# Performance work log

Hardware: AMD Instinct MI355X
Metric: run time of the kernel (lower is better)

Reference implementation:

```python
import jax, jax.numpy as jnp
import numpy as np

C = 128          # in_channels
NODE_NUM = 8192  # number of unique source nodes this step
D = 64           # max_member_num (fixed degree -> neighbor_bool all True)
E = NODE_NUM * D # total gathered neighbor slots
N_TOTAL = 200000 # total nodes in graph
NEG_SLOPE = 0.2


def setup_inputs() -> dict:
    key = jax.random.key(0)
    ks = jax.random.split(key, 8)
    node_features = jax.random.normal(ks[0], (N_TOTAL, C), jnp.float32)
    memory = jax.random.normal(ks[1], (N_TOTAL, C), jnp.float32)
    sc = 1.0 / np.sqrt(C)
    W_max = jax.random.normal(ks[2], (C, C), jnp.float32) * sc
    b_max = jnp.zeros((C,), jnp.float32)
    W_score = jax.random.normal(ks[3], (2 * C, 1), jnp.float32) * (1.0 / np.sqrt(2 * C))
    b_score = jnp.zeros((1,), jnp.float32)
    W_fit = jax.random.normal(ks[4], (C, 1), jnp.float32) * sc
    b_fit = jnp.zeros((1,), jnp.float32)
    neighbors = jax.random.randint(ks[5], (E,), 0, N_TOTAL)  # gathered neighbor node ids
    seg = jnp.repeat(jnp.arange(NODE_NUM), D)                # index_source_nodes (segment ids)
    return dict(node_features=node_features, memory=memory, W_max=W_max, b_max=b_max,
                W_score=W_score, b_score=b_score, W_fit=W_fit, b_fit=b_fit,
                neighbors=neighbors, seg=seg)


def reference(node_features, memory, W_max, b_max, W_score, b_score, W_fit, b_fit, neighbors, seg):
    # gather: features + detached memory per neighbor slot  [E, C]
    nbr = node_features[neighbors] + jax.lax.stop_gradient(memory[neighbors])
    # scatter_max per source node, then linear + re-gather duplication
    max_feature = jax.ops.segment_max(nbr, seg, num_segments=NODE_NUM)      # [node_num, C]
    max_lin = max_feature @ W_max + b_max                                    # [node_num, C]
    dup = max_lin[seg]                                                       # [E, C]
    # attention score over concat(center_max, neighbor)
    s = jnp.concatenate([dup, nbr], axis=-1) @ W_score + b_score             # [E, 1]
    s = jnp.where(s >= 0, s, NEG_SLOPE * s)                                  # leaky_relu
    # segment softmax over neighbors of each source node
    smax = jax.ops.segment_max(s, seg, num_segments=NODE_NUM)[seg]
    ex = jnp.exp(s - smax)
    denom = jax.ops.segment_sum(ex, seg, num_segments=NODE_NUM)[seg]
    score = ex / denom                                                       # [E, 1]
    # masked scatter into fixed [node_num, max_member_num] tensor (full mask -> reshape)
    score_tensor = score.reshape(NODE_NUM, D)
    # scatter_add pooling of score-weighted neighbor features
    cluster_feature = jax.ops.segment_sum(nbr * score, seg, num_segments=NODE_NUM)  # [node_num, C]
    # community fitness via linear score calculator + sigmoid
    fitness = jax.nn.sigmoid(cluster_feature @ W_fit + b_fit).reshape(-1)    # [node_num]
    return cluster_feature, score_tensor, fitness
```

## Files before the change

kernel.cpp:

```cpp
#include <hip/hip_runtime.h>
#include <hip/hip_fp16.h>
#include <math.h>

#define C_DIM 128
#define DEG 64
#define NEG_SLOPE 0.2f

typedef float nfloat4 __attribute__((ext_vector_type(4)));

__global__ __launch_bounds__(256)
void fuse_sum_half_kernel(const nfloat4* __restrict__ nf4,
                          const nfloat4* __restrict__ mem4,
                          nfloat4* __restrict__ sumh, long n8,
                          const float* __restrict__ W_max,
                          const float* __restrict__ b_max,
                          const float* __restrict__ W_score,
                          const float* __restrict__ b_score,
                          float* __restrict__ combo) {
    const long stride = (long)gridDim.x * 256;
    for (long i = (long)blockIdx.x * 256 + threadIdx.x; i < n8; i += stride) {
        const nfloat4 a0 = __builtin_nontemporal_load(nf4 + 2 * i);
        const nfloat4 a1 = __builtin_nontemporal_load(nf4 + 2 * i + 1);
        const nfloat4 b0 = __builtin_nontemporal_load(mem4 + 2 * i);
        const nfloat4 b1 = __builtin_nontemporal_load(mem4 + 2 * i + 1);
        const nfloat4 s0 = a0 + b0;
        const nfloat4 s1 = a1 + b1;
        __half2 h[4];
        h[0] = __floats2half2_rn(s0.x, s0.y);
        h[1] = __floats2half2_rn(s0.z, s0.w);
        h[2] = __floats2half2_rn(s1.x, s1.y);
        h[3] = __floats2half2_rn(s1.z, s1.w);
        sumh[i] = *(const nfloat4*)h;
    }
    if (blockIdx.x == 0) {
        const int c = threadIdx.x;
        __shared__ float red[C_DIM];
        if (c < C_DIM) {
            float acc = 0.f;
            #pragma unroll 4
            for (int k = 0; k < C_DIM; ++k)
                acc += W_max[c * C_DIM + k] * W_score[k];
            combo[c] = acc;
            red[c] = b_max[c] * W_score[c];
        }
        __syncthreads();
        for (int off = 64; off > 0; off >>= 1) {
            if (c < off) red[c] += red[c + off];
            __syncthreads();
        }
        if (c == 0) combo[C_DIM] = red[0] + b_score[0];
    }
}

__global__ __launch_bounds__(256)
void detector_half_kernel(const float4* __restrict__ sum4,
                          const float* __restrict__ W_score,
                          const float* __restrict__ W_fit,
                          const float* __restrict__ b_fit,
                          const int* __restrict__ neighbors,
                          const float* __restrict__ combo,
                          float* __restrict__ out_cf,
                          float* __restrict__ out_score,
                          float* __restrict__ out_fit) {
    __shared__ float4 red4[256][2];
    __shared__ float  chan[C_DIM];
    __shared__ float  s_raw[DEG];
    __shared__ float  sc[DEG];

    const int tid = threadIdx.x;
    const int n   = blockIdx.x;
    const int q   = tid & 15;
    const int g   = tid >> 4;

    const int4 nb = ((const int4*)(neighbors + n * DEG))[g];
    const int ids[4] = {nb.x, nb.y, nb.z, nb.w};

    const float4 wsb0 = ((const float4*)(W_score + C_DIM))[2 * q];
    const float4 wsb1 = ((const float4*)(W_score + C_DIM))[2 * q + 1];

    float4 vh[4];
    float mx[8];
    #pragma unroll
    for (int k = 0; k < 8; ++k) mx[k] = -INFINITY;

    #pragma unroll
    for (int i = 0; i < 4; ++i) {
        const long node = ids[i];
        const float4 hv = sum4[node * 16 + q];
        vh[i] = hv;
        const __half2* hp = (const __half2*)&hv;
        const float2 f0 = __half22float2(hp[0]);
        const float2 f1 = __half22float2(hp[1]);
        const float2 f2 = __half22float2(hp[2]);
        const float2 f3 = __half22float2(hp[3]);
        mx[0] = fmaxf(mx[0], f0.x); mx[1] = fmaxf(mx[1], f0.y);
        mx[2] = fmaxf(mx[2], f1.x); mx[3] = fmaxf(mx[3], f1.y);
        mx[4] = fmaxf(mx[4], f2.x); mx[5] = fmaxf(mx[5], f2.y);
        mx[6] = fmaxf(mx[6], f3.x); mx[7] = fmaxf(mx[7], f3.y);
        float p = f0.x * wsb0.x + f0.y * wsb0.y + f1.x * wsb0.z + f1.y * wsb0.w
                + f2.x * wsb1.x + f2.y * wsb1.y + f3.x * wsb1.z + f3.y * wsb1.w;
        p += __shfl_xor(p, 1);
        p += __shfl_xor(p, 2);
        p += __shfl_xor(p, 4);
        p += __shfl_xor(p, 8);
        if (q == 0) s_raw[g * 4 + i] = p;
    }
    asm volatile("" ::: "memory");

    red4[tid][0] = make_float4(mx[0], mx[1], mx[2], mx[3]);
    red4[tid][1] = make_float4(mx[4], mx[5], mx[6], mx[7]);
    __syncthreads();

    const float* rp = (const float*)red4;
    if (tid < C_DIM) {
        const int ch = tid >> 3;
        const int k  = tid & 7;
        float f = rp[(0 * 16 + ch) * 8 + k];
        #pragma unroll
        for (int g2 = 1; g2 < 16; ++g2)
            f = fmaxf(f, rp[(g2 * 16 + ch) * 8 + k]);
        chan[tid] = f * combo[tid];
    }
    __syncthreads();

    if (tid < DEG) {
        float t1 = chan[tid] + chan[tid + 64];
        #pragma unroll
        for (int msk = 1; msk <= 32; msk <<= 1)
            t1 += __shfl_xor(t1, msk);
        t1 += combo[C_DIM];
        float s = t1 + s_raw[tid];
        s = (s >= 0.f) ? s : NEG_SLOPE * s;
        float m = s;
        #pragma unroll
        for (int msk = 1; msk <= 32; msk <<= 1)
            m = fmaxf(m, __shfl_xor(m, msk));
        const float ex = __expf(s - m);
        float d = ex;
        #pragma unroll
        for (int msk = 1; msk <= 32; msk <<= 1)
            d += __shfl_xor(d, msk);
        const float sv = ex / d;
        sc[tid] = sv;
        out_score[n * DEG + tid] = sv;
    }
    __syncthreads();

    float acc[8] = {0.f, 0.f, 0.f, 0.f, 0.f, 0.f, 0.f, 0.f};
    #pragma unroll
    for (int i = 0; i < 4; ++i) {
        const float w = sc[g * 4 + i];
        const __half2* hp = (const __half2*)&vh[i];
        const float2 f0 = __half22float2(hp[0]);
        const float2 f1 = __half22float2(hp[1]);
        const float2 f2 = __half22float2(hp[2]);
        const float2 f3 = __half22float2(hp[3]);
        acc[0] += f0.x * w; acc[1] += f0.y * w;
        acc[2] += f1.x * w; acc[3] += f1.y * w;
        acc[4] += f2.x * w; acc[5] += f2.y * w;
        acc[6] += f3.x * w; acc[7] += f3.y * w;
    }
    __syncthreads();
    red4[tid][0] = make_float4(acc[0], acc[1], acc[2], acc[3]);
    red4[tid][1] = make_float4(acc[4], acc[5], acc[6], acc[7]);
    __syncthreads();

    if (tid < C_DIM) {
        const int ch = tid >> 3;
        const int k  = tid & 7;
        float f = 0.f;
        #pragma unroll
        for (int g2 = 0; g2 < 16; ++g2)
            f += rp[(g2 * 16 + ch) * 8 + k];
        out_cf[(long)n * C_DIM + tid] = f;
        chan[tid] = f * W_fit[tid];
    }
    __syncthreads();

    if (tid < DEG) {
        float t = chan[tid] + chan[tid + 64];
        #pragma unroll
        for (int msk = 1; msk <= 32; msk <<= 1)
            t += __shfl_xor(t, msk);
        if (tid == 0)
            out_fit[n] = 1.f / (1.f + __expf(-(t + b_fit[0])));
    }
}

__global__ void precompute_kernel(const float* __restrict__ W_max,
                                  const float* __restrict__ b_max,
                                  const float* __restrict__ W_score,
                                  const float* __restrict__ b_score,
                                  float* __restrict__ combo) {
    const int c = threadIdx.x;
    float acc = 0.f;
    for (int k = 0; k < C_DIM; ++k)
        acc += W_max[c * C_DIM + k] * W_score[k];
    combo[c] = acc;
    __shared__ float red[C_DIM];
    red[c] = b_max[c] * W_score[c];
    __syncthreads();
    for (int off = 64; off > 0; off >>= 1) {
        if (c < off) red[c] += red[c + off];
        __syncthreads();
    }
    if (c == 0) combo[C_DIM] = red[0] + b_score[0];
}

__global__ __launch_bounds__(256)
void detector_f32_kernel(const float* __restrict__ nf,
                         const float* __restrict__ mem,
                         const float* __restrict__ W_score,
                         const float* __restrict__ W_fit,
                         const float* __restrict__ b_fit,
                         const int* __restrict__ neighbors,
                         const float* __restrict__ combo,
                         float* __restrict__ out_cf,
                         float* __restrict__ out_score,
                         float* __restrict__ out_fit) {
    __shared__ float4 red[256];
    __shared__ float  s_raw[DEG];
    __shared__ float  sc[DEG];
    __shared__ float  t1_sh;

    const int tid = threadIdx.x;
    const int n   = blockIdx.x;
    const int q   = tid & 31;
    const int g   = tid >> 5;

    const int4* nb4 = (const int4*)(neighbors + n * DEG + g * 8);
    const int4 nba = nb4[0];
    const int4 nbb = nb4[1];
    const int ids[8] = {nba.x, nba.y, nba.z, nba.w, nbb.x, nbb.y, nbb.z, nbb.w};
    const float4 wsb = ((const float4*)(W_score + C_DIM))[q];
    const float4* nf4  = (const float4*)nf;
    const float4* mem4 = (const float4*)mem;

    float4 v[8];
    float4 mx = make_float4(-INFINITY, -INFINITY, -INFINITY, -INFINITY);
    #pragma unroll
    for (int i = 0; i < 8; ++i) {
        const long node = ids[i];
        float4 vv = nf4[node * 32 + q];
        const float4 b = mem4[node * 32 + q];
        vv.x += b.x; vv.y += b.y; vv.z += b.z; vv.w += b.w;
        v[i] = vv;
        mx.x = fmaxf(mx.x, vv.x); mx.y = fmaxf(mx.y, vv.y);
        mx.z = fmaxf(mx.z, vv.z); mx.w = fmaxf(mx.w, vv.w);
        float p = vv.x * wsb.x + vv.y * wsb.y + vv.z * wsb.z + vv.w * wsb.w;
        p += __shfl_xor(p, 1); p += __shfl_xor(p, 2); p += __shfl_xor(p, 4);
        p += __shfl_xor(p, 8); p += __shfl_xor(p, 16);
        if (q == 0) s_raw[g * 8 + i] = p;
    }
    asm volatile("" ::: "memory");
    red[tid] = mx;
    __syncthreads();
    if (tid < 32) {
        float4 f = red[tid];
        #pragma unroll
        for (int r = 1; r < 8; ++r) {
            const float4 o = red[tid + 32 * r];
            f.x = fmaxf(f.x, o.x); f.y = fmaxf(f.y, o.y);
            f.z = fmaxf(f.z, o.z); f.w = fmaxf(f.w, o.w);
        }
        const float4 wc = ((const float4*)combo)[tid];
        float t1 = f.x * wc.x + f.y * wc.y + f.z * wc.z + f.w * wc.w;
        t1 += __shfl_xor(t1, 1); t1 += __shfl_xor(t1, 2); t1 += __shfl_xor(t1, 4);
        t1 += __shfl_xor(t1, 8); t1 += __shfl_xor(t1, 16);
        if (tid == 0) t1_sh = t1 + combo[C_DIM];
    }
    __syncthreads();
    if (tid < DEG) {
        float s = t1_sh + s_raw[tid];
        s = (s >= 0.f) ? s : NEG_SLOPE * s;
        float m = s;
        #pragma unroll
        for (int msk = 1; msk <= 32; msk <<= 1) m = fmaxf(m, __shfl_xor(m, msk));
        const float ex = __expf(s - m);
        float d = ex;
        #pragma unroll
        for (int msk = 1; msk <= 32; msk <<= 1) d += __shfl_xor(d, msk);
        const float sv = ex / d;
        sc[tid] = sv;
        out_score[n * DEG + tid] = sv;
    }
    __syncthreads();
    float4 acc = make_float4(0.f, 0.f, 0.f, 0.f);
    #pragma unroll
    for (int i = 0; i < 8; ++i) {
        const float w = sc[g * 8 + i];
        acc.x += v[i].x * w; acc.y += v[i].y * w;
        acc.z += v[i].z * w; acc.w += v[i].w * w;
    }
    red[tid] = acc;
    __syncthreads();
    if (tid < 32) {
        float4 f = red[tid];
        #pragma unroll
        for (int r = 1; r < 8; ++r) {
            const float4 o = red[tid + 32 * r];
            f.x += o.x; f.y += o.y; f.z += o.z; f.w += o.w;
        }
        ((float4*)(out_cf + (long)n * C_DIM))[tid] = f;
        const float4 wf = ((const float4*)W_fit)[tid];
        float fp = f.x * wf.x + f.y * wf.y + f.z * wf.z + f.w * wf.w;
        fp += __shfl_xor(fp, 1); fp += __shfl_xor(fp, 2); fp += __shfl_xor(fp, 4);
        fp += __shfl_xor(fp, 8); fp += __shfl_xor(fp, 16);
        if (tid == 0)
            out_fit[n] = 1.f / (1.f + __expf(-(fp + b_fit[0])));
    }
}

extern "C" void kernel_launch(void* const* d_in, const int* in_sizes, int n_in,
                              void* d_out, int out_size, void* d_ws, size_t ws_size,
                              hipStream_t stream) {
    const float* node_features = (const float*)d_in[0];
    const float* memory        = (const float*)d_in[1];
    const float* W_max         = (const float*)d_in[2];
    const float* b_max         = (const float*)d_in[3];
    const float* W_score       = (const float*)d_in[4];
    const float* b_score       = (const float*)d_in[5];
    const float* W_fit         = (const float*)d_in[6];
    const float* b_fit         = (const float*)d_in[7];
    const int*   neighbors     = (const int*)d_in[8];

    const long n_elem = (long)in_sizes[0];
    const int  nodes  = in_sizes[8] / DEG;
    const long n8     = n_elem / 8;

    float* combo = (float*)d_ws;
    __half* sumh = (__half*)(combo + 512);
    const size_t need = 512 * sizeof(float) + (size_t)n_elem * sizeof(__half);

    float* out_cf    = (float*)d_out;
    float* out_score = out_cf + (long)nodes * C_DIM;
    float* out_fit   = out_score + (long)nodes * DEG;

    if (ws_size >= need) {
        fuse_sum_half_kernel<<<2048, 256, 0, stream>>>(
            (const nfloat4*)node_features, (const nfloat4*)memory,
            (nfloat4*)sumh, n8, W_max, b_max, W_score, b_score, combo);
        detector_half_kernel<<<nodes, 256, 0, stream>>>(
            (const float4*)sumh, W_score, W_fit, b_fit, neighbors, combo,
            out_cf, out_score, out_fit);
    } else {
        precompute_kernel<<<1, C_DIM, 0, stream>>>(W_max, b_max, W_score,
                                                   b_score, combo);
        detector_f32_kernel<<<nodes, 256, 0, stream>>>(
            node_features, memory, W_score, W_fit, b_fit, neighbors, combo,
            out_cf, out_score, out_fit);
    }
}
```

Before: 263.3 us.

## Process two source nodes per block and widen the fp16 pre-sum kernel

The detector kernel now handles two source nodes per 256-thread block, issuing all eight gathers per thread before any compute and combining the reduction stages for both nodes, so fewer barriers are paid per node. The pre-sum kernel drops its grid-stride loop and launches one thread per 16 floats, each doing eight nontemporal loads and two 16-byte stores. The aim is more memory-level parallelism in the random gather and less per-node synchronisation. It costs more registers and shared memory per block, and the fast path now requires an even node count and an element count divisible by 16.

```diff
diff --git a/kernel.cpp b/kernel.cpp
--- a/kernel.cpp
+++ b/kernel.cpp
@@ -11,26 +11,35 @@
 __global__ __launch_bounds__(256)
 void fuse_sum_half_kernel(const nfloat4* __restrict__ nf4,
                           const nfloat4* __restrict__ mem4,
-                          nfloat4* __restrict__ sumh, long n8,
+                          nfloat4* __restrict__ sumh4, long n16,
                           const float* __restrict__ W_max,
                           const float* __restrict__ b_max,
                           const float* __restrict__ W_score,
                           const float* __restrict__ b_score,
                           float* __restrict__ combo) {
-    const long stride = (long)gridDim.x * 256;
-    for (long i = (long)blockIdx.x * 256 + threadIdx.x; i < n8; i += stride) {
-        const nfloat4 a0 = __builtin_nontemporal_load(nf4 + 2 * i);
-        const nfloat4 a1 = __builtin_nontemporal_load(nf4 + 2 * i + 1);
-        const nfloat4 b0 = __builtin_nontemporal_load(mem4 + 2 * i);
-        const nfloat4 b1 = __builtin_nontemporal_load(mem4 + 2 * i + 1);
-        const nfloat4 s0 = a0 + b0;
-        const nfloat4 s1 = a1 + b1;
-        __half2 h[4];
-        h[0] = __floats2half2_rn(s0.x, s0.y);
-        h[1] = __floats2half2_rn(s0.z, s0.w);
-        h[2] = __floats2half2_rn(s1.x, s1.y);
-        h[3] = __floats2half2_rn(s1.z, s1.w);
-        sumh[i] = *(const nfloat4*)h;
+    const long idx = (long)blockIdx.x * 256 + threadIdx.x;
+    if (idx < n16) {
+        const long b = idx * 4;
+        nfloat4 a0 = __builtin_nontemporal_load(nf4 + b);
+        nfloat4 a1 = __builtin_nontemporal_load(nf4 + b + 1);
+        nfloat4 a2 = __builtin_nontemporal_load(nf4 + b + 2);
+        nfloat4 a3 = __builtin_nontemporal_load(nf4 + b + 3);
+        nfloat4 m0 = __builtin_nontemporal_load(mem4 + b);
+        nfloat4 m1 = __builtin_nontemporal_load(mem4 + b + 1);
+        nfloat4 m2 = __builtin_nontemporal_load(mem4 + b + 2);
+        nfloat4 m3 = __builtin_nontemporal_load(mem4 + b + 3);
+        const nfloat4 s0 = a0 + m0, s1 = a1 + m1, s2 = a2 + m2, s3 = a3 + m3;
+        __half2 h0[4], h1[4];
+        h0[0] = __floats2half2_rn(s0.x, s0.y);
+        h0[1] = __floats2half2_rn(s0.z, s0.w);
+        h0[2] = __floats2half2_rn(s1.x, s1.y);
+        h0[3] = __floats2half2_rn(s1.z, s1.w);
+        h1[0] = __floats2half2_rn(s2.x, s2.y);
+        h1[1] = __floats2half2_rn(s2.z, s2.w);
+        h1[2] = __floats2half2_rn(s3.x, s3.y);
+        h1[3] = __floats2half2_rn(s3.z, s3.w);
+        sumh4[idx * 2]     = *(const nfloat4*)h0;
+        sumh4[idx * 2 + 1] = *(const nfloat4*)h1;
     }
     if (blockIdx.x == 0) {
         const int c = threadIdx.x;
@@ -53,83 +62,92 @@
 }
 
 __global__ __launch_bounds__(256)
-void detector_half_kernel(const float4* __restrict__ sum4,
-                          const float* __restrict__ W_score,
-                          const float* __restrict__ W_fit,
-                          const float* __restrict__ b_fit,
-                          const int* __restrict__ neighbors,
-                          const float* __restrict__ combo,
-                          float* __restrict__ out_cf,
-                          float* __restrict__ out_score,
-                          float* __restrict__ out_fit) {
-    __shared__ float4 red4[256][2];
-    __shared__ float  chan[C_DIM];
-    __shared__ float  s_raw[DEG];
-    __shared__ float  sc[DEG];
+void detector_half2_kernel(const float4* __restrict__ sum4,
+                           const float* __restrict__ W_score,
+                           const float* __restrict__ W_fit,
+                           const float* __restrict__ b_fit,
+                           const int* __restrict__ neighbors,
+                           const float* __restrict__ combo,
+                           float* __restrict__ out_cf,
+                           float* __restrict__ out_score,
+                           float* __restrict__ out_fit) {
+    __shared__ float4 red4[2][256][2];
+    __shared__ float  chan[2][C_DIM];
+    __shared__ float  s_raw[2][DEG];
+    __shared__ float  sc[2][DEG];
 
     const int tid = threadIdx.x;
-    const int n   = blockIdx.x;
+    const int n0  = blockIdx.x * 2;
     const int q   = tid & 15;
     const int g   = tid >> 4;
 
-    const int4 nb = ((const int4*)(neighbors + n * DEG))[g];
-    const int ids[4] = {nb.x, nb.y, nb.z, nb.w};
+    int4 nb[2];
+    nb[0] = ((const int4*)(neighbors + (long)n0 * DEG))[g];
+    nb[1] = ((const int4*)(neighbors + (long)(n0 + 1) * DEG))[g];
 
     const float4 wsb0 = ((const float4*)(W_score + C_DIM))[2 * q];
     const float4 wsb1 = ((const float4*)(W_score + C_DIM))[2 * q + 1];
 
-    float4 vh[4];
-    float mx[8];
+    float4 vh[2][4];
+    {
+        const int ids0[4] = {nb[0].x, nb[0].y, nb[0].z, nb[0].w};
+        const int ids1[4] = {nb[1].x, nb[1].y, nb[1].z, nb[1].w};
+        #pragma unroll
+        for (int i = 0; i < 4; ++i) vh[0][i] = sum4[(long)ids0[i] * 16 + q];
+        #pragma unroll
+        for (int i = 0; i < 4; ++i) vh[1][i] = sum4[(long)ids1[i] * 16 + q];
+    }
+    asm volatile("" ::: "memory");
+
     #pragma unroll
-    for (int k = 0; k < 8; ++k) mx[k] = -INFINITY;
-
-    #pragma unroll
-    for (int i = 0; i < 4; ++i) {
-        const long node = ids[i];
-        const float4 hv = sum4[node * 16 + q];
-        vh[i] = hv;
-        const __half2* hp = (const __half2*)&hv;
-        const float2 f0 = __half22float2(hp[0]);
-        const float2 f1 = __half22float2(hp[1]);
-        const float2 f2 = __half22float2(hp[2]);
-        const float2 f3 = __half22float2(hp[3]);
-        mx[0] = fmaxf(mx[0], f0.x); mx[1] = fmaxf(mx[1], f0.y);
-        mx[2] = fmaxf(mx[2], f1.x); mx[3] = fmaxf(mx[3], f1.y);
-        mx[4] = fmaxf(mx[4], f2.x); mx[5] = fmaxf(mx[5], f2.y);
-        mx[6] = fmaxf(mx[6], f3.x); mx[7] = fmaxf(mx[7], f3.y);
-        float p = f0.x * wsb0.x + f0.y * wsb0.y + f1.x * wsb0.z + f1.y * wsb0.w
-                + f2.x * wsb1.x + f2.y * wsb1.y + f3.x * wsb1.z + f3.y * wsb1.w;
-        p += __shfl_xor(p, 1);
-        p += __shfl_xor(p, 2);
-        p += __shfl_xor(p, 4);
-        p += __shfl_xor(p, 8);
-        if (q == 0) s_raw[g * 4 + i] = p;
-    }
-    asm volatile("" ::: "memory");
-
-    red4[tid][0] = make_float4(mx[0], mx[1], mx[2], mx[3]);
-    red4[tid][1] = make_float4(mx[4], mx[5], mx[6], mx[7]);
-    __syncthreads();
-
-    const float* rp = (const float*)red4;
-    if (tid < C_DIM) {
-        const int ch = tid >> 3;
-        const int k  = tid & 7;
-        float f = rp[(0 * 16 + ch) * 8 + k];
+    for (int p = 0; p < 2; ++p) {
+        float mx[8];
+        #pragma unroll
+        for (int k = 0; k < 8; ++k) mx[k] = -INFINITY;
+        #pragma unroll
+        for (int i = 0; i < 4; ++i) {
+            const __half2* hp = (const __half2*)&vh[p][i];
+            const float2 f0 = __half22float2(hp[0]);
+            const float2 f1 = __half22float2(hp[1]);
+            const float2 f2 = __half22float2(hp[2]);
+            const float2 f3 = __half22float2(hp[3]);
+            mx[0] = fmaxf(mx[0], f0.x); mx[1] = fmaxf(mx[1], f0.y);
+            mx[2] = fmaxf(mx[2], f1.x); mx[3] = fmaxf(mx[3], f1.y);
+            mx[4] = fmaxf(mx[4], f2.x); mx[5] = fmaxf(mx[5], f2.y);
+            mx[6] = fmaxf(mx[6], f3.x); mx[7] = fmaxf(mx[7], f3.y);
+            float pd = f0.x * wsb0.x + f0.y * wsb0.y + f1.x * wsb0.z + f1.y * wsb0.w
+                     + f2.x * wsb1.x + f2.y * wsb1.y + f3.x * wsb1.z + f3.y * wsb1.w;
+            pd += __shfl_xor(pd, 1);
+            pd += __shfl_xor(pd, 2);
+            pd += __shfl_xor(pd, 4);
+            pd += __shfl_xor(pd, 8);
+            if (q == 0) s_raw[p][g * 4 + i] = pd;
+        }
+        red4[p][tid][0] = make_float4(mx[0], mx[1], mx[2], mx[3]);
+        red4[p][tid][1] = make_float4(mx[4], mx[5], mx[6], mx[7]);
+    }
+    __syncthreads();
+
+    {
+        const int p = tid >> 7, c = tid & 127;
+        const int ch = c >> 3, k = c & 7;
+        const float* rp = (const float*)red4[p];
+        float f = rp[ch * 8 + k];
         #pragma unroll
         for (int g2 = 1; g2 < 16; ++g2)
             f = fmaxf(f, rp[(g2 * 16 + ch) * 8 + k]);
-        chan[tid] = f * combo[tid];
-    }
-    __syncthreads();
-
-    if (tid < DEG) {
-        float t1 = chan[tid] + chan[tid + 64];
+        chan[p][c] = f * combo[c];
+    }
+    __syncthreads();
+
+    if (tid < 128) {
+        const int p = tid >> 6, slot = tid & 63;
+        float t1 = chan[p][slot] + chan[p][slot + 64];
         #pragma unroll
         for (int msk = 1; msk <= 32; msk <<= 1)
             t1 += __shfl_xor(t1, msk);
         t1 += combo[C_DIM];
-        float s = t1 + s_raw[tid];
+        float s = t1 + s_raw[p][slot];
         s = (s >= 0.f) ? s : NEG_SLOPE * s;
         float m = s;
         #pragma unroll
@@ -141,49 +159,53 @@
         for (int msk = 1; msk <= 32; msk <<= 1)
             d += __shfl_xor(d, msk);
         const float sv = ex / d;
-        sc[tid] = sv;
-        out_score[n * DEG + tid] = sv;
-    }
-    __syncthreads();
-
-    float acc[8] = {0.f, 0.f, 0.f, 0.f, 0.f, 0.f, 0.f, 0.f};
+        sc[p][slot] = sv;
+        out_score[(long)(n0 + p) * DEG + slot] = sv;
+    }
+    __syncthreads();
+
     #pragma unroll
-    for (int i = 0; i < 4; ++i) {
-        const float w = sc[g * 4 + i];
-        const __half2* hp = (const __half2*)&vh[i];
-        const float2 f0 = __half22float2(hp[0]);
-        const float2 f1 = __half22float2(hp[1]);
-        const float2 f2 = __half22float2(hp[2]);
-        const float2 f3 = __half22float2(hp[3]);
-        acc[0] += f0.x * w; acc[1] += f0.y * w;
-        acc[2] += f1.x * w; acc[3] += f1.y * w;
-        acc[4] += f2.x * w; acc[5] += f2.y * w;
-        acc[6] += f3.x * w; acc[7] += f3.y * w;
-    }
-    __syncthreads();
-    red4[tid][0] = make_float4(acc[0], acc[1], acc[2], acc[3]);
-    red4[tid][1] = make_float4(acc[4], acc[5], acc[6], acc[7]);
-    __syncthreads();
-
-    if (tid < C_DIM) {
-        const int ch = tid >> 3;
-        const int k  = tid & 7;
+    for (int p = 0; p < 2; ++p) {
+        float acc[8] = {0.f, 0.f, 0.f, 0.f, 0.f, 0.f, 0.f, 0.f};
+        #pragma unroll
+        for (int i = 0; i < 4; ++i) {
+            const float w = sc[p][g * 4 + i];
+            const __half2* hp = (const __half2*)&vh[p][i];
+            const float2 f0 = __half22float2(hp[0]);
+            const float2 f1 = __half22float2(hp[1]);
+            const float2 f2 = __half22float2(hp[2]);
+            const float2 f3 = __half22float2(hp[3]);
+            acc[0] += f0.x * w; acc[1] += f0.y * w;
+            acc[2] += f1.x * w; acc[3] += f1.y * w;
+            acc[4] += f2.x * w; acc[5] += f2.y * w;
+            acc[6] += f3.x * w; acc[7] += f3.y * w;
+        }
+        red4[p][tid][0] = make_float4(acc[0], acc[1], acc[2], acc[3]);
+        red4[p][tid][1] = make_float4(acc[4], acc[5], acc[6], acc[7]);
+    }
+    __syncthreads();
+
+    {
+        const int p = tid >> 7, c = tid & 127;
+        const int ch = c >> 3, k = c & 7;
+        const float* rp = (const float*)red4[p];
         float f = 0.f;
         #pragma unroll
         for (int g2 = 0; g2 < 16; ++g2)
             f += rp[(g2 * 16 + ch) * 8 + k];
-        out_cf[(long)n * C_DIM + tid] = f;
-        chan[tid] = f * W_fit[tid];
-    }
-    __syncthreads();
-
-    if (tid < DEG) {
-        float t = chan[tid] + chan[tid + 64];
+        out_cf[(long)(n0 + p) * C_DIM + c] = f;
+        chan[p][c] = f * W_fit[c];
+    }
+    __syncthreads();
+
+    if (tid < 128) {
+        const int p = tid >> 6, slot = tid & 63;
+        float t = chan[p][slot] + chan[p][slot + 64];
         #pragma unroll
         for (int msk = 1; msk <= 32; msk <<= 1)
             t += __shfl_xor(t, msk);
-        if (tid == 0)
-            out_fit[n] = 1.f / (1.f + __expf(-(t + b_fit[0])));
+        if (slot == 0)
+            out_fit[n0 + p] = 1.f / (1.f + __expf(-(t + b_fit[0])));
     }
 }
 
@@ -326,7 +348,7 @@
 
     const long n_elem = (long)in_sizes[0];
     const int  nodes  = in_sizes[8] / DEG;
-    const long n8     = n_elem / 8;
+    const long n16    = (n_elem + 15) / 16;
 
     float* combo = (float*)d_ws;
     __half* sumh = (__half*)(combo + 512);
@@ -336,11 +358,12 @@
     float* out_score = out_cf + (long)nodes * C_DIM;
     float* out_fit   = out_score + (long)nodes * DEG;
 
-    if (ws_size >= need) {
-        fuse_sum_half_kernel<<<2048, 256, 0, stream>>>(
+    if (ws_size >= need && (n_elem % 16) == 0 && (nodes % 2) == 0) {
+        const int blocks = (int)((n16 + 255) / 256);
+        fuse_sum_half_kernel<<<blocks, 256, 0, stream>>>(
             (const nfloat4*)node_features, (const nfloat4*)memory,
-            (nfloat4*)sumh, n8, W_max, b_max, W_score, b_score, combo);
-        detector_half_kernel<<<nodes, 256, 0, stream>>>(
+            (nfloat4*)sumh, n16, W_max, b_max, W_score, b_score, combo);
+        detector_half2_kernel<<<nodes / 2, 256, 0, stream>>>(
             (const float4*)sumh, W_score, W_fit, b_fit, neighbors, combo,
             out_cf, out_score, out_fit);
     } else {
```

Result: slower. 270.8 us (+2.9%).
